# Kernel tuning notes

Hardware: AMD Instinct MI355X
Metric: run time of the kernel (lower is better)

## Reference

```python
import jax, jax.numpy as jnp
import numpy as np

B, C, Hf, T = 8, 2, 257, 2048
D_IN = C * Hf          # 514
DM = 256               # d_model
NL = 4                 # n_layers
N = 32                 # S4D complex state size (d_state=64 -> N=32 complex modes)


def setup_inputs() -> dict:
    key = jax.random.key(0)
    ks = jax.random.split(key, 16)
    sc_in = 1.0 / np.sqrt(D_IN)
    sc_dm = 1.0 / np.sqrt(DM)
    inp = {}
    inp['x'] = jax.random.normal(ks[0], (B, C, Hf, T, 2), dtype=jnp.float32)
    # complex encoder (d_input -> d_model)
    inp['enc_Wr'] = jax.random.normal(ks[1], (DM, D_IN), dtype=jnp.float32) * sc_in
    inp['enc_Wi'] = jax.random.normal(ks[2], (DM, D_IN), dtype=jnp.float32) * sc_in
    inp['enc_br'] = jnp.zeros((DM,), jnp.float32)
    inp['enc_bi'] = jnp.zeros((DM,), jnp.float32)
    # per-layer S4D kernel params (stacked over layers)
    lo, hi = np.log(0.001), np.log(0.1)
    inp['log_dt'] = jax.random.uniform(ks[3], (NL, DM), dtype=jnp.float32) * (hi - lo) + lo
    inp['log_A_real'] = jnp.full((NL, DM, N), np.log(0.5), dtype=jnp.float32)
    inp['A_imag'] = jnp.broadcast_to(np.pi * jnp.arange(N, dtype=jnp.float32), (NL, DM, N)) + 0.0
    inp['C_r'] = jax.random.normal(ks[4], (NL, DM, N), dtype=jnp.float32)
    inp['C_i'] = jax.random.normal(ks[5], (NL, DM, N), dtype=jnp.float32)
    inp['D'] = jax.random.normal(ks[6], (NL, DM), dtype=jnp.float32)
    # per-layer complex pointwise output linear (d_model -> d_model)
    inp['out_Wr'] = jax.random.normal(ks[7], (NL, DM, DM), dtype=jnp.float32) * sc_dm
    inp['out_Wi'] = jax.random.normal(ks[8], (NL, DM, DM), dtype=jnp.float32) * sc_dm
    inp['out_br'] = jnp.zeros((NL, DM), jnp.float32)
    inp['out_bi'] = jnp.zeros((NL, DM), jnp.float32)
    # per-layer complex LayerNorm (separate real/imag affine)
    inp['ln_gamma_r'] = jnp.ones((NL, DM), jnp.float32)
    inp['ln_gamma_i'] = jnp.ones((NL, DM), jnp.float32)
    inp['ln_beta_r'] = jnp.zeros((NL, DM), jnp.float32)
    inp['ln_beta_i'] = jnp.zeros((NL, DM), jnp.float32)
    # complex decoder (d_model -> d_output = c*h)
    inp['dec_Wr'] = jax.random.normal(ks[9], (D_IN, DM), dtype=jnp.float32) * sc_dm
    inp['dec_Wi'] = jax.random.normal(ks[10], (D_IN, DM), dtype=jnp.float32) * sc_dm
    inp['dec_br'] = jnp.zeros((D_IN,), jnp.float32)
    inp['dec_bi'] = jnp.zeros((D_IN,), jnp.float32)
    return inp


def _clinear(xr, xi, Wr, Wi, br, bi):
    # complex linear: (xr + i xi) @ (Wr + i Wi)^T + (br + i bi)
    yr = xr @ Wr.T - xi @ Wi.T + br
    yi = xi @ Wr.T + xr @ Wi.T + bi
    return yr, yi


def _layernorm_ch(v, g, b, eps=1e-5):
    # normalize over channel axis 1 of (B, H, T)
    m = v.mean(axis=1, keepdims=True)
    var = ((v - m) ** 2).mean(axis=1, keepdims=True)
    return (v - m) / jnp.sqrt(var + eps) * g[None, :, None] + b[None, :, None]


def _forward(x, enc_Wr, enc_Wi, enc_br, enc_bi, log_dt, log_A_real, A_imag,
             C_r, C_i, D, out_Wr, out_Wi, out_br, out_bi,
             ln_gamma_r, ln_gamma_i, ln_beta_r, ln_beta_i,
             dec_Wr, dec_Wi, dec_br, dec_bi):
    b, c, h, T, _ = x.shape
    xf = x.reshape(b, c * h, T, 2)
    xf = jnp.swapaxes(xf, 1, 2)               # (b, T, c*h, 2)
    zr, zi = _clinear(xf[..., 0], xf[..., 1], enc_Wr, enc_Wi, enc_br, enc_bi)  # (b, T, DM)
    zr = jnp.swapaxes(zr, -1, -2)             # (b, DM, T)
    zi = jnp.swapaxes(zi, -1, -2)
    tgrid = jnp.arange(T, dtype=jnp.float32)
    n_layers = log_dt.shape[0]
    for l in range(n_layers):
        # ---- ComplexS4D kernel (diagonal SSM, ZOH-like discretization) ----
        dt = jnp.exp(log_dt[l])[:, None]                        # (H,1)
        A = -jnp.exp(log_A_real[l]) + 1j * A_imag[l]            # (H,N) complex
        dtA = A * dt                                            # (H,N)
        Ct = (C_r[l] + 1j * C_i[l]) * (jnp.exp(dtA) - 1.0) / A  # (H,N)
        K = jnp.einsum('hn,hnl->hl', Ct, jnp.exp(dtA[:, :, None] * tgrid))  # complex (H,T)
        # ---- complex FFT causal convolution ----
        u = zr + 1j * zi                                        # (b,H,T)
        y = jnp.fft.ifft(jnp.fft.fft(u, 2 * T) * jnp.fft.fft(K, 2 * T)[None])[..., :T]
        y = y + D[l][None, :, None] * u                         # skip connection
        yr = jax.nn.gelu(y.real)
        yi = jax.nn.gelu(y.imag)
        # ---- complex pointwise output linear ----
        orr = jnp.einsum('bht,gh->bgt', yr, out_Wr[l]) - jnp.einsum('bht,gh->bgt', yi, out_Wi[l]) + out_br[l][None, :, None]
        oii = jnp.einsum('bht,gh->bgt', yi, out_Wr[l]) + jnp.einsum('bht,gh->bgt', yr, out_Wi[l]) + out_bi[l][None, :, None]
        # residual + post-norm (prenorm=False), complex LayerNorm over d_model
        zr = _layernorm_ch(zr + orr, ln_gamma_r[l], ln_beta_r[l])
        zi = _layernorm_ch(zi + oii, ln_gamma_i[l], ln_beta_i[l])
    zr = jnp.swapaxes(zr, -1, -2)             # (b, T, DM)
    zi = jnp.swapaxes(zi, -1, -2)
    dr, di = _clinear(zr, zi, dec_Wr, dec_Wi, dec_br, dec_bi)  # (b, T, c*h)
    dr = jnp.swapaxes(dr, 1, 2)               # (b, c*h, T)
    di = jnp.swapaxes(di, 1, 2)
    return jnp.stack([dr, di], axis=-1).reshape(b, c, h, T, 2)


def reference(x, enc_Wr, enc_Wi, enc_br, enc_bi, log_dt, log_A_real, A_imag,
              C_r, C_i, D, out_Wr, out_Wi, out_br, out_bi,
              ln_gamma_r, ln_gamma_i, ln_beta_r, ln_beta_i,
              dec_Wr, dec_Wi, dec_br, dec_bi):
    return _forward(x, enc_Wr, enc_Wi, enc_br, enc_bi, log_dt, log_A_real, A_imag,
                    C_r, C_i, D, out_Wr, out_Wi, out_br, out_bi,
                    ln_gamma_r, ln_gamma_i, ln_beta_r, ln_beta_i,
                    dec_Wr, dec_Wi, dec_br, dec_bi)
```

## Files before the change

kernel.cpp:

```cpp
#include <hip/hip_runtime.h>
#include <cstddef>
#include <cstdint>


typedef __attribute__((ext_vector_type(8))) short short8;
typedef __attribute__((ext_vector_type(4))) float float4v;

__device__ __forceinline__ unsigned short f2bf(float f) {
    union { float f; unsigned u; } v; v.f = f;
    const unsigned r = v.u + 0x7fffu + ((v.u >> 16) & 1u);
    return (unsigned short)(r >> 16);
}

__device__ __forceinline__ float gelu_tanh(float x) {
    const float x3 = x * x * x;
    const float v  = 0.7978845608028654f * (x + 0.044715f * x3);
    const float e  = __expf(2.f * v);
    const float th = 1.f - 2.f / (e + 1.f);
    return 0.5f * x * (1.f + th);
}

template<int CTL>
__device__ __forceinline__ float dppadd(float x) {
    union { float f; int i; } a, r;
    a.f = x;
    r.i = __builtin_amdgcn_update_dpp(a.i, a.i, CTL, 0xF, 0xF, true);
    return x + r.f;
}
#define DPP_XOR1 0xB1
#define DPP_XOR2 0x4E

#define ASYNC_COPY16(gp, lp) __builtin_amdgcn_global_load_lds( \
    (const __attribute__((address_space(1))) unsigned int*)(gp), \
    (__attribute__((address_space(3))) unsigned int*)(lp), 16, 0, 0)

__global__ __launch_bounds__(256) void buildw_k(
    const float* __restrict__ Wr, const float* __restrict__ Wi,
    unsigned short* __restrict__ A, int G, int H, int Hoff, int Kp, int Mp)
{
    const long long i = (long long)blockIdx.x * 256 + threadIdx.x;
    if (i >= (long long)Mp * Kp) return;
    const int m = (int)(i / Kp), k = (int)(i % Kp);
    float val = 0.f;
    if (m < 2 * G) {
        const int ri = m >= G;
        const int g = m - ri * G;
        const int blk = k >= Hoff;
        const int hh = k - blk * Hoff;
        if (hh < H) {
            const float wr = Wr[(size_t)g * H + hh];
            const float wi = Wi[(size_t)g * H + hh];
            val = ri ? (blk ? wr : wi) : (blk ? -wi : wr);
        }
    }
    A[i] = f2bf(val);
}

__global__ __launch_bounds__(256) void buildwL_k(
    const float* __restrict__ Wr0, const float* __restrict__ Wi0,
    unsigned short* __restrict__ A0)
{
    const int l = blockIdx.y;
    const float* Wr = Wr0 + (size_t)l * 65536;
    const float* Wi = Wi0 + (size_t)l * 65536;
    unsigned short* A = A0 + (size_t)l * 262144;
    const int i = blockIdx.x * 256 + threadIdx.x;
    const int m = i >> 9, k = i & 511;
    const int ri = m >= 256;
    const int g = m & 255;
    const int blk = k >> 8;
    const int hh = k & 255;
    const float wr = Wr[(size_t)g * 256 + hh];
    const float wi = Wi[(size_t)g * 256 + hh];
    const float val = ri ? (blk ? wr : wi) : (blk ? -wi : wr);
    A[i] = f2bf(val);
}

__global__ __launch_bounds__(256) void build_bias_k(
    const float* __restrict__ br, const float* __restrict__ bi,
    float* __restrict__ bias, int G)
{
    const int i = blockIdx.x * 256 + threadIdx.x;
    if (i < G) bias[i] = br[i];
    else if (i < 2 * G) bias[i] = bi[i - G];
}

__global__ __launch_bounds__(256) void build_biasL_k(
    const float* __restrict__ br0, const float* __restrict__ bi0,
    float* __restrict__ bias0)
{
    const int l = blockIdx.y;
    const int i = blockIdx.x * 256 + threadIdx.x;
    const float* br = br0 + l * 256;
    const float* bi = bi0 + l * 256;
    float* bias = bias0 + l * 512;
    if (i < 256) bias[i] = br[i];
    else bias[i] = bi[i - 256];
}

__global__ __launch_bounds__(256) void packx_k(const float* __restrict__ x,
                                               unsigned short* __restrict__ xp)
{
    const int t0 = blockIdx.x * 64, d0 = blockIdx.y * 64, b = blockIdx.z;
    __shared__ unsigned short tr_[64][72];
    __shared__ unsigned short ti_[64][72];
    const int tid = threadIdx.x;
    const int tp = tid & 31, dl0 = tid >> 5;
#pragma unroll
    for (int p = 0; p < 8; ++p) {
        const int d = dl0 + p * 8;
        const int gd = d0 + d;
        float4 v = make_float4(0.f, 0.f, 0.f, 0.f);
        if (gd < 514) v = *(const float4*)(x + (((size_t)b * 514 + gd) * 2048 + t0 + tp * 2) * 2);
        tr_[tp * 2 + 0][d] = f2bf(v.x); ti_[tp * 2 + 0][d] = f2bf(v.y);
        tr_[tp * 2 + 1][d] = f2bf(v.z); ti_[tp * 2 + 1][d] = f2bf(v.w);
    }
    __syncthreads();
    const int dc = tid & 7;
    const int kloc = d0 + dc * 8;
    if (kloc < 528) {
#pragma unroll
        for (int p = 0; p < 2; ++p) {
            const int t = (tid >> 3) + p * 32;
            const size_t rowb = ((size_t)b * 2048 + t0 + t) * 1056;
            *(short8*)&xp[rowb + kloc]       = *(const short8*)&tr_[t][dc * 8];
            *(short8*)&xp[rowb + 528 + kloc] = *(const short8*)&ti_[t][dc * 8];
        }
    }
}

template<int SRC32>
__global__ __launch_bounds__(256) void tr_k(const void* __restrict__ src,
                                            unsigned short* __restrict__ dst)
{
    const int t0 = blockIdx.x * 64, k0 = blockIdx.y * 64, b = blockIdx.z;
    __shared__ unsigned short tile[64][72];
    const int tid = threadIdx.x;
    if (SRC32) {
        const float* sf = (const float*)src;
        const int tp = tid & 31, kl0 = tid >> 5;
#pragma unroll
        for (int p = 0; p < 8; ++p) {
            const int kl = kl0 + p * 8;
            const float2 v = *(const float2*)(sf + ((size_t)b * 512 + k0 + kl) * 2048 + t0 + tp * 2);
            tile[tp * 2 + 0][kl] = f2bf(v.x);
            tile[tp * 2 + 1][kl] = f2bf(v.y);
        }
    } else {
        const unsigned short* su = (const unsigned short*)src;
        const int toct = tid & 7, kl0 = tid >> 3;
#pragma unroll
        for (int p = 0; p < 2; ++p) {
            const int kl = kl0 + p * 32;
            const short8 v = *(const short8*)(su + ((size_t)b * 512 + k0 + kl) * 2048 + t0 + toct * 8);
#pragma unroll
            for (int j = 0; j < 8; ++j) tile[toct * 8 + j][kl] = ((const unsigned short*)&v)[j];
        }
    }
    __syncthreads();
    const int dc = tid & 7;
#pragma unroll
    for (int p = 0; p < 2; ++p) {
        const int t = (tid >> 3) + p * 32;
        *(short8*)&dst[((size_t)b * 2048 + t0 + t) * 512 + k0 + dc * 8] = *(const short8*)&tile[t][dc * 8];
    }
}

template<int MODE>
__global__ __launch_bounds__(256, 2) void mgemm_k(
    const unsigned short* __restrict__ A, const float* __restrict__ bias,
    const unsigned short* __restrict__ Bm, float* __restrict__ out,
    int M, int Kp)
{
    __shared__ unsigned short As[4096];
    __shared__ unsigned short Bs[4096];
    const int tid = threadIdx.x;
    const int w = tid >> 6, lane = tid & 63;
    const int m0 = blockIdx.x * 128, t0 = blockIdx.y * 128, b = blockIdx.z;
    const int wm = w & 1, wn = w >> 1;

    const unsigned short* Ab = A + (size_t)m0 * Kp;
    const unsigned short* Bb = Bm + ((size_t)b * 2048 + t0) * Kp;

    const int c0 = w * 64 + lane;
    const int r0 = c0 >> 2, q0 = (c0 & 3) * 8;
    const int c1 = c0 + 256;
    const int r1 = c1 >> 2, q1 = (c1 & 3) * 8;
    unsigned short* As0 = &As[(size_t)(w * 64) * 8];
    unsigned short* As1 = &As[(size_t)(w * 64 + 256) * 8];
    unsigned short* Bs0 = &Bs[(size_t)(w * 64) * 8];
    unsigned short* Bs1 = &Bs[(size_t)(w * 64 + 256) * 8];

    float4v acc[4][4];
#pragma unroll
    for (int i = 0; i < 4; ++i)
#pragma unroll
        for (int j = 0; j < 4; ++j) acc[i][j] = (float4v){0.f, 0.f, 0.f, 0.f};

    const int arow = wm * 64 + (lane & 15);
    const int brow = wn * 64 + (lane & 15);
    const int kq = (lane >> 4) * 8;

    for (int k0 = 0; k0 < Kp; k0 += 32) {
        ASYNC_COPY16(Ab + (size_t)r0 * Kp + k0 + q0, As0);
        ASYNC_COPY16(Ab + (size_t)r1 * Kp + k0 + q1, As1);
        ASYNC_COPY16(Bb + (size_t)r0 * Kp + k0 + q0, Bs0);
        ASYNC_COPY16(Bb + (size_t)r1 * Kp + k0 + q1, Bs1);
        __syncthreads();
        short8 af[4], bf[4];
#pragma unroll
        for (int i = 0; i < 4; ++i) af[i] = *(const short8*)&As[(arow + i * 16) * 32 + kq];
#pragma unroll
        for (int j = 0; j < 4; ++j) bf[j] = *(const short8*)&Bs[(brow + j * 16) * 32 + kq];
#pragma unroll
        for (int i = 0; i < 4; ++i)
#pragma unroll
            for (int j = 0; j < 4; ++j)
                acc[i][j] = __builtin_amdgcn_mfma_f32_16x16x32_bf16(af[i], bf[j], acc[i][j], 0, 0, 0);
        __syncthreads();
    }

    const int col = lane & 15;
    const int rq = (lane >> 4) * 4;
#pragma unroll
    for (int i = 0; i < 4; ++i) {
        const int mloc = wm * 64 + i * 16 + rq;
#pragma unroll
        for (int r = 0; r < 4; ++r) {
            const int m = m0 + mloc + r;
            if (MODE == 1 && m >= M) continue;
            const float bs = bias[m];
#pragma unroll
            for (int j = 0; j < 4; ++j) {
                const int t = t0 + wn * 64 + j * 16 + col;
                const float vv = acc[i][j][r] + bs;
                if (MODE == 0) {
                    out[((size_t)b * 512 + m) * 2048 + t] = vv;
                } else {
                    const int comp = m >= 514;
                    const int g = m - 514 * comp;
                    out[(((size_t)b * 514 + g) * 2048 + t) * 2 + comp] = vv;
                }
            }
        }
    }
}

__global__ __launch_bounds__(512, 2) void mgemmln_k(
    const unsigned short* __restrict__ A, const float* __restrict__ bias,
    const unsigned short* __restrict__ Bm, float* __restrict__ z,
    const float* __restrict__ gamr, const float* __restrict__ gami,
    const float* __restrict__ betr, const float* __restrict__ beti, int l)
{
    __shared__ unsigned short Bs[64][520];
    __shared__ float biasS[512], gamS[512], betS[512];
    __shared__ float sred[8][64][2];
    __shared__ float sstat[2][64][2];
    const int tid = threadIdx.x;
    const int w = tid >> 6, lane = tid & 63;
    const int t0g = blockIdx.x * 64, b = blockIdx.y;

    {
        const unsigned char* src = (const unsigned char*)(Bm + ((size_t)b * 2048 + t0g) * 512);
        unsigned char* dstb = (unsigned char*)&Bs[0][0];
#pragma unroll
        for (int p = 0; p < 8; ++p) {
            const int go = p * 8192 + tid * 16;
            const int t = go >> 10, off = go & 1023;
            *(short8*)(dstb + t * 1040 + off) = *(const short8*)(src + t * 1024 + off);
        }
        const int m = tid, g = m & 255, comp = m >> 8;
        biasS[m] = bias[m];
        gamS[m] = (comp ? gami : gamr)[l * 256 + g];
        betS[m] = (comp ? beti : betr)[l * 256 + g];
    }
    __syncthreads();

    float4v acc[4][4];
#pragma unroll
    for (int i = 0; i < 4; ++i)
#pragma unroll
        for (int j = 0; j < 4; ++j) acc[i][j] = (float4v){0.f, 0.f, 0.f, 0.f};

    const int brow = lane & 15;
    const int kq8 = (lane >> 4) * 8;
    const unsigned short* Ab = A + ((size_t)(w * 64 + brow)) * 512 + kq8;
    const unsigned char* BsB = (const unsigned char*)&Bs[0][0];

#define LOADF(af_, bf_, k0_) do {                                              \
    _Pragma("unroll")                                                          \
    for (int i = 0; i < 4; ++i)                                                \
        af_[i] = *(const short8*)(Ab + (size_t)i * 16 * 512 + (k0_));          \
    _Pragma("unroll")                                                          \
    for (int j = 0; j < 4; ++j)                                                \
        bf_[j] = *(const short8*)(BsB + (j * 16 + brow) * 1040 + ((k0_) + kq8) * 2); \
} while (0)
#define MFMAS(af_, bf_) do {                                                   \
    _Pragma("unroll")                                                          \
    for (int i = 0; i < 4; ++i)                                                \
        _Pragma("unroll")                                                      \
        for (int j = 0; j < 4; ++j)                                            \
            acc[i][j] = __builtin_amdgcn_mfma_f32_16x16x32_bf16(af_[i], bf_[j], acc[i][j], 0, 0, 0); \
} while (0)

    {
        short8 afA[4], bfA[4], afB[4], bfB[4];
        LOADF(afA, bfA, 0);
#pragma unroll 1
        for (int kk = 0; kk < 16; kk += 2) {
            LOADF(afB, bfB, kk * 32 + 32);
            MFMAS(afA, bfA);
            if (kk + 2 < 16) LOADF(afA, bfA, kk * 32 + 64);
            MFMAS(afB, bfB);
        }
    }
#undef LOADF
#undef MFMAS

    const int q4 = (lane >> 4) * 4;
    float4 b4[4], g4[4], e4[4];
#pragma unroll
    for (int i = 0; i < 4; ++i) {
        const int m0 = w * 64 + i * 16 + q4;
        b4[i] = *(const float4*)&biasS[m0];
        g4[i] = *(const float4*)&gamS[m0];
        e4[i] = *(const float4*)&betS[m0];
    }

    float s1[4], s2[4];
#pragma unroll
    for (int j = 0; j < 4; ++j) { s1[j] = 0.f; s2[j] = 0.f; }
#pragma unroll
    for (int j = 0; j < 4; ++j) {
        const int t = t0g + j * 16 + brow;
#pragma unroll
        for (int i = 0; i < 4; ++i) {
            const int m = w * 64 + i * 16 + q4;
            const float* zp = &z[((size_t)b * 512 + m) * 2048 + t];
            const float bb[4] = {b4[i].x, b4[i].y, b4[i].z, b4[i].w};
#pragma unroll
            for (int r = 0; r < 4; ++r) {
                const float v = acc[i][j][r] + bb[r] + zp[(size_t)r * 2048];
                acc[i][j][r] = v;
                s1[j] += v; s2[j] += v * v;
            }
        }
    }
#pragma unroll
    for (int j = 0; j < 4; ++j) {
        s1[j] += __shfl_xor(s1[j], 16); s2[j] += __shfl_xor(s2[j], 16);
        s1[j] += __shfl_xor(s1[j], 32); s2[j] += __shfl_xor(s2[j], 32);
    }
    if (lane < 16) {
#pragma unroll
        for (int j = 0; j < 4; ++j) {
            sred[w][j * 16 + lane][0] = s1[j];
            sred[w][j * 16 + lane][1] = s2[j];
        }
    }
    __syncthreads();
    if (tid < 128) {
        const int t = tid & 63, comp = tid >> 6;
        float S1 = 0.f, S2 = 0.f;
#pragma unroll
        for (int w2 = 0; w2 < 4; ++w2) {
            S1 += sred[comp * 4 + w2][t][0];
            S2 += sred[comp * 4 + w2][t][1];
        }
        const float mn = S1 * (1.f / 256.f);
        const float var = S2 * (1.f / 256.f) - mn * mn;
        sstat[comp][t][0] = mn;
        sstat[comp][t][1] = rsqrtf(var + 1e-5f);
    }
    __syncthreads();
    const int comp = w >> 2;
#pragma unroll
    for (int j = 0; j < 4; ++j) {
        const int tl = j * 16 + brow;
        const float mn = sstat[comp][tl][0], rs = sstat[comp][tl][1];
        const int t = t0g + tl;
#pragma unroll
        for (int i = 0; i < 4; ++i) {
            const int m = w * 64 + i * 16 + q4;
            float* zp = &z[((size_t)b * 512 + m) * 2048 + t];
            const float gg[4] = {g4[i].x, g4[i].y, g4[i].z, g4[i].w};
            const float ee[4] = {e4[i].x, e4[i].y, e4[i].z, e4[i].w};
#pragma unroll
            for (int r = 0; r < 4; ++r)
                zp[(size_t)r * 2048] = (acc[i][j][r] - mn) * rs * gg[r] + ee[r];
        }
    }
}

__global__ __launch_bounds__(256, 4) void s4scan_k(
    const float* __restrict__ z, unsigned short* __restrict__ y,
    const float* __restrict__ log_dt, const float* __restrict__ log_A_real,
    const float* __restrict__ A_imag, const float* __restrict__ C_r,
    const float* __restrict__ C_i, const float* __restrict__ Dsk, int l)
{
    const int h = blockIdx.x, b = blockIdx.y;
    const int tid = threadIdx.x;
    const int lane = tid & 63, wv = tid >> 6;
    __shared__ float2 wsh[32], csh[32];
    __shared__ float dsh;
    __shared__ float2 us[64][33];
    __shared__ __align__(16) unsigned char uni[64 * 33 * 8];
    float2 (*vsh2)[33] = (float2(*)[33])uni;
    float2 (*ys)[33]   = (float2(*)[33])uni;

    if (tid < 32) {
        const size_t pidx = ((size_t)l * 256 + h) * 32 + tid;
        const float dt = __expf(log_dt[l * 256 + h]);
        const float Ar = -__expf(log_A_real[pidx]);
        const float Ai = A_imag[pidx];
        const float er = __expf(Ar * dt);
        float sv, cv;
        __sincosf(Ai * dt, &sv, &cv);
        const float wr = er * cv, wi = er * sv;
        const float den = 1.f / (Ar * Ar + Ai * Ai);
        const float nr = wr - 1.f, ni = wi;
        const float qr = (nr * Ar + ni * Ai) * den;
        const float qi = (ni * Ar - nr * Ai) * den;
        const float cr = C_r[pidx], ci = C_i[pidx];
        wsh[tid] = make_float2(wr, wi);
        csh[tid] = make_float2(cr * qr - ci * qi, cr * qi + ci * qr);
    }
    if (tid == 32) dsh = Dsk[l * 256 + h];

    const int c0q = tid >> 2, t0q = (tid & 3) * 8;
    {
        const float* zrp = z + ((size_t)b * 512 + h) * 2048 + tid * 8;
        const float* zip = zrp + 256 * 2048;
        const float4 r0 = *(const float4*)zrp, r1 = *(const float4*)(zrp + 4);
        const float4 i0 = *(const float4*)zip, i1 = *(const float4*)(zip + 4);
        float2* up = &us[c0q][t0q];
        up[0] = make_float2(r0.x, i0.x); up[1] = make_float2(r0.y, i0.y);
        up[2] = make_float2(r0.z, i0.z); up[3] = make_float2(r0.w, i0.w);
        up[4] = make_float2(r1.x, i1.x); up[5] = make_float2(r1.y, i1.y);
        up[6] = make_float2(r1.z, i1.z); up[7] = make_float2(r1.w, i1.w);
    }
    __syncthreads();

    {
        float2 w8[8], x8[8];
#pragma unroll
        for (int j = 0; j < 8; ++j) {
            w8[j] = wsh[wv * 8 + j];
            x8[j] = make_float2(0.f, 0.f);
        }
#pragma unroll 8
        for (int tt = 0; tt < 32; ++tt) {
            const float2 u = us[lane][tt];
#pragma unroll
            for (int j = 0; j < 8; ++j) {
                const float nxr = __builtin_fmaf(w8[j].x, x8[j].x, __builtin_fmaf(-w8[j].y, x8[j].y, u.x));
                const float nxi = __builtin_fmaf(w8[j].x, x8[j].y, __builtin_fmaf(w8[j].y, x8[j].x, u.y));
                x8[j].x = nxr; x8[j].y = nxi;
            }
        }
#pragma unroll
        for (int j = 0; j < 8; ++j) {
            float fr = w8[j].x, fi = w8[j].y;
#pragma unroll
            for (int s = 0; s < 5; ++s) { const float a2 = fr * fr - fi * fi, b2 = 2.f * fr * fi; fr = a2; fi = b2; }
            float qrv = x8[j].x, qiv = x8[j].y, pr = fr, pi = fi;
#pragma unroll
            for (int s = 0; s < 6; ++s) {
                const int d = 1 << s;
                const float sr = __shfl_up(qrv, (unsigned)d);
                const float si = __shfl_up(qiv, (unsigned)d);
                if (lane >= d) {
                    qrv += pr * sr - pi * si;
                    qiv += pr * si + pi * sr;
                }
                const float a2 = pr * pr - pi * pi, b2 = 2.f * pr * pi;
                pr = a2; pi = b2;
            }
            float vr = __shfl_up(qrv, 1u);
            float vi = __shfl_up(qiv, 1u);
            if (lane == 0) { vr = 0.f; vi = 0.f; }
            vsh2[lane][wv * 8 + j] = make_float2(vr, vi);
        }
    }
    __syncthreads();

    {
        const int q = tid & 3;
        float2 w8[8], c8[8], s8[8];
#pragma unroll
        for (int j = 0; j < 8; ++j) {
            const int n = q * 8 + j;
            w8[j] = wsh[n];
            c8[j] = csh[n];
            s8[j] = vsh2[c0q][n];
        }
        __syncthreads();
#pragma unroll 4
        for (int tt = 0; tt < 32; ++tt) {
            const float2 u = us[c0q][tt];
            float pyr = 0.f, pyi = 0.f;
#pragma unroll
            for (int j = 0; j < 8; ++j) {
                const float nsr = __builtin_fmaf(w8[j].x, s8[j].x, __builtin_fmaf(-w8[j].y, s8[j].y, u.x));
                const float nsi = __builtin_fmaf(w8[j].x, s8[j].y, __builtin_fmaf(w8[j].y, s8[j].x, u.y));
                s8[j].x = nsr; s8[j].y = nsi;
                pyr = __builtin_fmaf(c8[j].x, nsr, __builtin_fmaf(-c8[j].y, nsi, pyr));
                pyi = __builtin_fmaf(c8[j].x, nsi, __builtin_fmaf(c8[j].y, nsr, pyi));
            }
            pyr = dppadd<DPP_XOR1>(pyr); pyr = dppadd<DPP_XOR2>(pyr);
            pyi = dppadd<DPP_XOR1>(pyi); pyi = dppadd<DPP_XOR2>(pyi);
            if (q == 0) ys[c0q][tt] = make_float2(pyr, pyi);
        }
    }
    __syncthreads();

    {
        const float dv = dsh;
        unsigned short* yrp = y + ((size_t)b * 512 + h) * 2048 + tid * 8;
        unsigned short* yip = yrp + 256 * 2048;
        short8 vr8, vi8;
#pragma unroll
        for (int j = 0; j < 8; ++j) {
            const float2 yv = ys[c0q][t0q + j];
            const float2 uv = us[c0q][t0q + j];
            ((unsigned short*)&vr8)[j] = f2bf(gelu_tanh(__builtin_fmaf(dv, uv.x, yv.x)));
            ((unsigned short*)&vi8)[j] = f2bf(gelu_tanh(__builtin_fmaf(dv, uv.y, yv.y)));
        }
        *(short8*)yrp = vr8;
        *(short8*)yip = vi8;
    }
}

extern "C" void kernel_launch(void* const* d_in, const int* in_sizes, int n_in,
                              void* d_out, int out_size, void* d_ws, size_t ws_size,
                              hipStream_t stream)
{
    const float* x        = (const float*)d_in[0];
    const float* enc_Wr   = (const float*)d_in[1];
    const float* enc_Wi   = (const float*)d_in[2];
    const float* enc_br   = (const float*)d_in[3];
    const float* enc_bi   = (const float*)d_in[4];
    const float* log_dt   = (const float*)d_in[5];
    const float* log_A_r  = (const float*)d_in[6];
    const float* A_imag   = (const float*)d_in[7];
    const float* C_r      = (const float*)d_in[8];
    const float* C_i      = (const float*)d_in[9];
    const float* Dp       = (const float*)d_in[10];
    const float* out_Wr   = (const float*)d_in[11];
    const float* out_Wi   = (const float*)d_in[12];
    const float* out_br   = (const float*)d_in[13];
    const float* out_bi   = (const float*)d_in[14];
    const float* ln_gr    = (const float*)d_in[15];
    const float* ln_gi    = (const float*)d_in[16];
    const float* ln_br    = (const float*)d_in[17];
    const float* ln_bi    = (const float*)d_in[18];
    const float* dec_Wr   = (const float*)d_in[19];
    const float* dec_Wi   = (const float*)d_in[20];
    const float* dec_br   = (const float*)d_in[21];
    const float* dec_bi   = (const float*)d_in[22];

    uint8_t* W = (uint8_t*)d_ws;
    float* z             = (float*)W;
    unsigned short* zp   = (unsigned short*)(W + 33554432);
    unsigned short* A_enc= (unsigned short*)(W + 50331648);
    unsigned short* A_lay= (unsigned short*)(W + 51412992);
    unsigned short* A_dec= (unsigned short*)(W + 53510144);
    float* b_enc         = (float*)(W + 54689792);
    float* b_lay         = (float*)(W + 54691840);
    float* b_dec         = (float*)(W + 54700032);

    unsigned short* y   = (unsigned short*)((uint8_t*)d_out + 33554432);
    unsigned short* yp  = (unsigned short*)((uint8_t*)d_out + 50331648);
    unsigned short* xp  = (unsigned short*)d_out;

    buildw_k<<<2112, 256, 0, stream>>>(enc_Wr, enc_Wi, A_enc, 256, 514, 528, 1056, 512);
    buildwL_k<<<dim3(1024, 4), 256, 0, stream>>>(out_Wr, out_Wi, A_lay);
    buildw_k<<<2304, 256, 0, stream>>>(dec_Wr, dec_Wi, A_dec, 514, 256, 256, 512, 1152);
    build_bias_k<<<2, 256, 0, stream>>>(enc_br, enc_bi, b_enc, 256);
    build_biasL_k<<<dim3(2, 4), 256, 0, stream>>>(out_br, out_bi, b_lay);
    build_bias_k<<<5, 256, 0, stream>>>(dec_br, dec_bi, b_dec, 514);

    packx_k<<<dim3(32, 9, 8), 256, 0, stream>>>(x, xp);
    mgemm_k<0><<<dim3(4, 16, 8), 256, 0, stream>>>(A_enc, b_enc, xp, z, 512, 1056);

    for (int l = 0; l < 4; ++l) {
        s4scan_k<<<dim3(256, 8), 256, 0, stream>>>(z, y, log_dt, log_A_r, A_imag, C_r, C_i, Dp, l);
        tr_k<0><<<dim3(32, 8, 8), 256, 0, stream>>>(y, yp);
        mgemmln_k<<<dim3(32, 8), 512, 0, stream>>>(A_lay + (size_t)l * 262144,
                                                   b_lay + l * 512, yp, z,
                                                   ln_gr, ln_gi, ln_br, ln_bi, l);
    }

    tr_k<1><<<dim3(32, 8, 8), 256, 0, stream>>>(z, zp);
    mgemm_k<1><<<dim3(9, 16, 8), 256, 0, stream>>>(A_dec, b_dec, zp, (float*)d_out, 1028, 512);
}
```

Measured before the change: 622.9 us.

## Fuse y transpose into layer GEMM load with XOR-swizzled LDS layout

Drops the separate per-layer transpose kernel that rewrote y (channel-major bf16) into time-major yp. mgemmln_k now reads y directly with coalesced 16-byte row loads and scatters the values transposed into LDS. It uses an XOR swizzle in place of row padding so the MFMA B-fragment reads avoid bank conflicts. This removes four kernel launches and a full read and write of the y buffer per layer, in exchange for scalar 2-byte LDS stores during the tile load.

Result: faster. 593.3 us (-4.8%).

```diff
diff --git a/kernel.cpp b/kernel.cpp
--- a/kernel.cpp
+++ b/kernel.cpp
@@ -129,33 +129,19 @@
     }
 }
 
-template<int SRC32>
-__global__ __launch_bounds__(256) void tr_k(const void* __restrict__ src,
-                                            unsigned short* __restrict__ dst)
+__global__ __launch_bounds__(256) void trz_k(const float* __restrict__ sf,
+                                             unsigned short* __restrict__ dst)
 {
     const int t0 = blockIdx.x * 64, k0 = blockIdx.y * 64, b = blockIdx.z;
     __shared__ unsigned short tile[64][72];
     const int tid = threadIdx.x;
-    if (SRC32) {
-        const float* sf = (const float*)src;
-        const int tp = tid & 31, kl0 = tid >> 5;
-#pragma unroll
-        for (int p = 0; p < 8; ++p) {
-            const int kl = kl0 + p * 8;
-            const float2 v = *(const float2*)(sf + ((size_t)b * 512 + k0 + kl) * 2048 + t0 + tp * 2);
-            tile[tp * 2 + 0][kl] = f2bf(v.x);
-            tile[tp * 2 + 1][kl] = f2bf(v.y);
-        }
-    } else {
-        const unsigned short* su = (const unsigned short*)src;
-        const int toct = tid & 7, kl0 = tid >> 3;
-#pragma unroll
-        for (int p = 0; p < 2; ++p) {
-            const int kl = kl0 + p * 32;
-            const short8 v = *(const short8*)(su + ((size_t)b * 512 + k0 + kl) * 2048 + t0 + toct * 8);
-#pragma unroll
-            for (int j = 0; j < 8; ++j) tile[toct * 8 + j][kl] = ((const unsigned short*)&v)[j];
-        }
+    const int tp = tid & 31, kl0 = tid >> 5;
+#pragma unroll
+    for (int p = 0; p < 8; ++p) {
+        const int kl = kl0 + p * 8;
+        const float2 v = *(const float2*)(sf + ((size_t)b * 512 + k0 + kl) * 2048 + t0 + tp * 2);
+        tile[tp * 2 + 0][kl] = f2bf(v.x);
+        tile[tp * 2 + 1][kl] = f2bf(v.y);
     }
     __syncthreads();
     const int dc = tid & 7;
@@ -252,22 +238,30 @@
     const float* __restrict__ gamr, const float* __restrict__ gami,
     const float* __restrict__ betr, const float* __restrict__ beti, int l)
 {
-    __shared__ unsigned short Bs[64][520];
+    __shared__ unsigned short Bs[64][512];
     __shared__ float biasS[512], gamS[512], betS[512];
     __shared__ float sred[8][64][2];
     __shared__ float sstat[2][64][2];
     const int tid = threadIdx.x;
     const int w = tid >> 6, lane = tid & 63;
     const int t0g = blockIdx.x * 64, b = blockIdx.y;
+    unsigned char* BsB = (unsigned char*)&Bs[0][0];
 
     {
-        const unsigned char* src = (const unsigned char*)(Bm + ((size_t)b * 2048 + t0g) * 512);
-        unsigned char* dstb = (unsigned char*)&Bs[0][0];
+        const unsigned short* ysrc = Bm + (size_t)b * 512 * 2048 + t0g;
+        const int tseg = lane & 7;
+        const int rloc = lane >> 3;
 #pragma unroll
         for (int p = 0; p < 8; ++p) {
-            const int go = p * 8192 + tid * 16;
-            const int t = go >> 10, off = go & 1023;
-            *(short8*)(dstb + t * 1040 + off) = *(const short8*)(src + t * 1024 + off);
+            const int krow = w * 8 + rloc + p * 64;
+            const short8 v = *(const short8*)(ysrc + (size_t)krow * 2048 + tseg * 8);
+#pragma unroll
+            for (int j = 0; j < 8; ++j) {
+                const int t = tseg * 8 + j;
+                const int mask = (((t & 7) ^ ((t >> 3) & 7)) << 4);
+                *(unsigned short*)(BsB + t * 1024 + ((krow * 2) ^ mask)) =
+                    ((const unsigned short*)&v)[j];
+            }
         }
         const int m = tid, g = m & 255, comp = m >> 8;
         biasS[m] = bias[m];
@@ -285,7 +279,13 @@
     const int brow = lane & 15;
     const int kq8 = (lane >> 4) * 8;
     const unsigned short* Ab = A + ((size_t)(w * 64 + brow)) * 512 + kq8;
-    const unsigned char* BsB = (const unsigned char*)&Bs[0][0];
+    int baseB[4], maskB[4];
+#pragma unroll
+    for (int j = 0; j < 4; ++j) {
+        const int t = j * 16 + brow;
+        baseB[j] = t * 1024;
+        maskB[j] = (((t & 7) ^ ((t >> 3) & 7)) << 4);
+    }
 
 #define LOADF(af_, bf_, k0_) do {                                              \
     _Pragma("unroll")                                                          \
@@ -293,7 +293,7 @@
         af_[i] = *(const short8*)(Ab + (size_t)i * 16 * 512 + (k0_));          \
     _Pragma("unroll")                                                          \
     for (int j = 0; j < 4; ++j)                                                \
-        bf_[j] = *(const short8*)(BsB + (j * 16 + brow) * 1040 + ((k0_) + kq8) * 2); \
+        bf_[j] = *(const short8*)(BsB + baseB[j] + ((((k0_) + kq8) * 2) ^ maskB[j])); \
 } while (0)
 #define MFMAS(af_, bf_) do {                                                   \
     _Pragma("unroll")                                                          \
@@ -570,7 +570,6 @@
     float* b_dec         = (float*)(W + 54700032);
 
     unsigned short* y   = (unsigned short*)((uint8_t*)d_out + 33554432);
-    unsigned short* yp  = (unsigned short*)((uint8_t*)d_out + 50331648);
     unsigned short* xp  = (unsigned short*)d_out;
 
     buildw_k<<<2112, 256, 0, stream>>>(enc_Wr, enc_Wi, A_enc, 256, 514, 528, 1056, 512);
@@ -585,12 +584,11 @@
 
     for (int l = 0; l < 4; ++l) {
         s4scan_k<<<dim3(256, 8), 256, 0, stream>>>(z, y, log_dt, log_A_r, A_imag, C_r, C_i, Dp, l);
-        tr_k<0><<<dim3(32, 8, 8), 256, 0, stream>>>(y, yp);
         mgemmln_k<<<dim3(32, 8), 512, 0, stream>>>(A_lay + (size_t)l * 262144,
-                                                   b_lay + l * 512, yp, z,
+                                                   b_lay + l * 512, y, z,
                                                    ln_gr, ln_gi, ln_br, ln_bi, l);
     }
 
-    tr_k<1><<<dim3(32, 8, 8), 256, 0, stream>>>(z, zp);
+    trz_k<<<dim3(32, 8, 8), 256, 0, stream>>>(z, zp);
     mgemm_k<1><<<dim3(9, 16, 8), 256, 0, stream>>>(A_dec, b_dec, zp, (float*)d_out, 1028, 512);
 }
```
